# Kernel optimization log

Measured on AMD Instinct MI355X. Metric: run time of the kernel, lower is better.

Reference implementation:

```python
import jax, jax.numpy as jnp
import numpy as np

B, T, N, C = 4, 2048, 4, 1024   # batch, seq, expansion_rate, hidden_dim
A = 8                            # max_lora_adapters
SINKHORN_ITERS = 20
EPS = 1e-05


def _logit(x):
    x = jnp.clip(x, 1e-06, 1.0 - 1e-06)
    return jnp.log(x) - jnp.log(1.0 - x)


def setup_inputs() -> dict:
    key = jax.random.key(0)
    ks = jax.random.split(key, 12)
    nC = N * C
    x = jax.random.normal(ks[0], (B, T, N, C), dtype=jnp.float32)
    adapter_indices = jax.random.randint(ks[1], (B,), 0, A)
    # Learned parameters (perturbed from the identity init so gradients are non-trivial)
    input_norm_weight = 1.0 + 0.02 * jax.random.normal(ks[2], (A, nC), dtype=jnp.float32)
    phi_pre = 0.02 * jax.random.normal(ks[3], (A, nC, N), dtype=jnp.float32)
    phi_post = 0.02 * jax.random.normal(ks[4], (A, nC, N), dtype=jnp.float32)
    phi_res = 0.02 * jax.random.normal(ks[5], (A, nC, N * N), dtype=jnp.float32)
    b_pre = _logit(jnp.float32(1.0 / N)) + 0.1 * jax.random.normal(ks[6], (A, N), dtype=jnp.float32)
    b_post = 0.1 * jax.random.normal(ks[7], (A, N), dtype=jnp.float32)
    b_res = 10.0 * jnp.eye(N, dtype=jnp.float32) + jax.random.normal(ks[8], (A, N, N), dtype=jnp.float32)
    alpha_pre = 1.0 + 0.1 * jax.random.normal(ks[9], (A,), dtype=jnp.float32)
    alpha_post = 1.0 + 0.1 * jax.random.normal(ks[10], (A,), dtype=jnp.float32)
    alpha_res = 1.0 + 0.1 * jax.random.normal(ks[11], (A,), dtype=jnp.float32)
    return {
        "x": x,
        "input_norm_weight": input_norm_weight,
        "phi_pre": phi_pre, "phi_post": phi_post, "phi_res": phi_res,
        "b_pre": b_pre, "b_post": b_post, "b_res": b_res,
        "alpha_pre": alpha_pre, "alpha_post": alpha_post, "alpha_res": alpha_res,
        "adapter_indices": adapter_indices,
    }


def _sinkhorn_knopp(M, iters):
    M = jnp.exp(M)
    def step(_, mat):
        mat = mat / mat.sum(axis=-1, keepdims=True)
        mat = mat / mat.sum(axis=-2, keepdims=True)
        return mat
    return jax.lax.fori_loop(0, iters, step, M)


def reference(x, input_norm_weight, phi_pre, phi_post, phi_res,
              b_pre, b_post, b_res, alpha_pre, alpha_post, alpha_res,
              adapter_indices):
    Bb, Tt, n, Cc = x.shape
    idx = adapter_indices.astype(jnp.int32)
    x_flat = x.reshape(Bb, Tt, n * Cc)
    # adapter-indexed RMSNorm
    w = input_norm_weight[idx]                                  # [B, nC]
    rms = jnp.sqrt(jnp.mean(x_flat ** 2, axis=-1, keepdims=True) + EPS)
    x_norm = w[:, None, :] * x_flat / rms                       # [B, T, nC]
    # pre: input-dependent aggregation weights H_pre
    pre_logits = jnp.einsum('btd,bdn->btn', x_norm, phi_pre[idx])
    H_pre = jax.nn.sigmoid(alpha_pre[idx][:, None, None] * pre_logits + b_pre[idx][:, None, :])
    x_agg = (H_pre[..., None] * x).sum(axis=-2)                 # [B, T, C]
    output = x_agg                                              # identity block between pre and post
    # post: distribution weights H_post and doubly-stochastic mixing M
    post_logits = jnp.einsum('btd,bdn->btn', x_norm, phi_post[idx])
    H_post = 2.0 * jax.nn.sigmoid(alpha_post[idx][:, None, None] * post_logits + b_post[idx][:, None, :])
    res_logits = jnp.einsum('btd,bdm->btm', x_norm, phi_res[idx]).reshape(Bb, Tt, n, n)
    tilde_H_res = alpha_res[idx][:, None, None, None] * res_logits + b_res[idx][:, None, :, :]
    M = _sinkhorn_knopp(tilde_H_res, SINKHORN_ITERS)            # [B, T, n, n]
    y_dist = H_post[..., None] * output[..., None, :]           # [B, T, n, C]
    x_mixed = jnp.einsum('btij,btjc->btic', M, x)               # [B, T, n, C]
    return x_mixed + y_dist
```

## Files before the change

kernel.cpp:

```cpp
#include <hip/hip_runtime.h>


#define BT 8192
#define NC 4096
#define NC4 1024
#define NT 32
#define TD 128

__global__ __launch_bounds__(256) void lora_connector_kernel(
    const float* __restrict__ x,
    const float* __restrict__ inw,
    const float* __restrict__ phi_pre,
    const float* __restrict__ phi_post,
    const float* __restrict__ phi_res,
    const float* __restrict__ b_pre,
    const float* __restrict__ b_post,
    const float* __restrict__ b_res,
    const float* __restrict__ alpha_pre,
    const float* __restrict__ alpha_post,
    const float* __restrict__ alpha_res,
    const int*   __restrict__ adapter_indices,
    float* __restrict__ out)
{
    const int tid = threadIdx.x;
    const int g   = tid & 3;
    const int l   = tid >> 2;
    const int wvid= tid >> 6;
    const int ln  = tid & 63;
    const int dl  = tid & 127;
    const int half= tid >> 7;
    const int blk = blockIdx.x;
    const int b   = blk >> 9;
    const int idx = adapter_indices[b];

    const float4* __restrict__ pp4 = (const float4*)(phi_pre  + (size_t)idx * (NC * 4));
    const float4* __restrict__ po4 = (const float4*)(phi_post + (size_t)idx * (NC * 4));
    const float4* __restrict__ pr4 = (const float4*)(phi_res  + (size_t)idx * (NC * 16));
    const float*  __restrict__ inwp = inw + (size_t)idx * NC + dl;
    const float*  __restrict__ xb   = x + (size_t)(blk * 4) * NC + dl;

    __shared__ float4 tileL[2][768];
    __shared__ float red[4][4][14];

    const float4* sg[3];
    int sstr[3];
    #pragma unroll
    for (int i = 0; i < 3; ++i) {
        const int c = wvid * 3 + i;
        const float4* bp; int off, str;
        if (c < 4) {
            bp  = (c < 2) ? pp4 : po4;
            off = ((c & 1) << 6) + ln;
            str = TD;
        } else {
            const int k = c - 4;
            bp  = pr4;
            off = ((((k & 1) << 6) + ln) << 2) + (k >> 1);
            str = TD * 4;
        }
        sg[i] = bp + off;
        sstr[i] = str;
    }

    #define STAGE_TILE(MT, BF)                                                   \
    {                                                                            \
        _Pragma("unroll")                                                        \
        for (int i = 0; i < 3; ++i) {                                            \
            __builtin_amdgcn_global_load_lds(                                    \
                (const __attribute__((address_space(1))) void*)(sg[i] + (size_t)(MT) * sstr[i]), \
                (__attribute__((address_space(3))) void*)&tileL[BF][((wvid * 3 + i) << 6) + ln], \
                16, 0, 0);                                                       \
        }                                                                        \
    }

    STAGE_TILE(0, 0);

    float acc[12][4];
    float ss[4];
    #pragma unroll
    for (int j = 0; j < 12; ++j) {
        acc[j][0] = 0.0f; acc[j][1] = 0.0f; acc[j][2] = 0.0f; acc[j][3] = 0.0f;
    }
    ss[0] = ss[1] = ss[2] = ss[3] = 0.0f;

    float xn[4], wn;
    #pragma unroll
    for (int j = 0; j < 4; ++j) xn[j] = xb[j * NC];
    wn = inwp[0];

    const int ba = half * 384 + dl;

    #pragma unroll 1
    for (int m = 0; m < NT; ++m) {
        const int bf = m & 1;
        __syncthreads();
        if (m < NT - 1) STAGE_TILE(m + 1, bf ^ 1);

        const float wv = wn;
        float s[4];
        #pragma unroll
        for (int j = 0; j < 4; ++j) {
            const float xv = xn[j];
            s[j] = xv * wv;
            ss[j] = fmaf(xv, xv, ss[j]);
        }
        if (m < NT - 1) {
            #pragma unroll
            for (int j = 0; j < 4; ++j) xn[j] = xb[j * NC + (m + 1) * TD];
            wn = inwp[(m + 1) * TD];
        }

        const float4 a = tileL[bf][ba];
        const float4 p = tileL[bf][ba + 128];
        const float4 r = tileL[bf][ba + 256];
        #pragma unroll
        for (int j = 0; j < 4; ++j) {
            acc[0][j]  = fmaf(s[j], a.x, acc[0][j]);
            acc[1][j]  = fmaf(s[j], a.y, acc[1][j]);
            acc[2][j]  = fmaf(s[j], a.z, acc[2][j]);
            acc[3][j]  = fmaf(s[j], a.w, acc[3][j]);
            acc[4][j]  = fmaf(s[j], p.x, acc[4][j]);
            acc[5][j]  = fmaf(s[j], p.y, acc[5][j]);
            acc[6][j]  = fmaf(s[j], p.z, acc[6][j]);
            acc[7][j]  = fmaf(s[j], p.w, acc[7][j]);
            acc[8][j]  = fmaf(s[j], r.x, acc[8][j]);
            acc[9][j]  = fmaf(s[j], r.y, acc[9][j]);
            acc[10][j] = fmaf(s[j], r.z, acc[10][j]);
            acc[11][j] = fmaf(s[j], r.w, acc[11][j]);
        }
    }

    float t12[13];
    #define RED4(V0, V1, V2, V3, DST)                                   \
    {                                                                   \
        const float u0 = (V0) + __shfl_xor((V0), 1);                    \
        const float u1 = (V1) + __shfl_xor((V1), 1);                    \
        const float u2 = (V2) + __shfl_xor((V2), 1);                    \
        const float u3 = (V3) + __shfl_xor((V3), 1);                    \
        const float r0 = (ln & 1) ? u1 : u0;                            \
        const float r1 = (ln & 1) ? u3 : u2;                            \
        const float w0 = r0 + __shfl_xor(r0, 2);                        \
        const float w1 = r1 + __shfl_xor(r1, 2);                        \
        float tv = (ln & 2) ? w1 : w0;                                  \
        tv += __shfl_xor(tv, 4);  tv += __shfl_xor(tv, 8);              \
        tv += __shfl_xor(tv, 16); tv += __shfl_xor(tv, 32);             \
        (DST) = tv;                                                     \
    }
    #pragma unroll
    for (int j = 0; j < 12; ++j)
        RED4(acc[j][0], acc[j][1], acc[j][2], acc[j][3], t12[j]);
    RED4(ss[0], ss[1], ss[2], ss[3], t12[12]);
    #undef RED4

    if (ln < 4) {
        #pragma unroll
        for (int j = 0; j < 13; ++j) red[wvid][ln][j] = t12[j];
    }
    __syncthreads();
    float tot[25];
    #pragma unroll
    for (int j = 0; j < 12; ++j) {
        tot[j]      = red[0][g][j] + red[1][g][j];
        tot[12 + j] = red[2][g][j] + red[3][g][j];
    }
    tot[24] = red[0][g][12] + red[1][g][12];

    const float inv_rms = rsqrtf(tot[24] * (1.0f / 4096.0f) + 1e-5f);
    const float apre  = alpha_pre[idx];
    const float apost = alpha_post[idx];
    const float ares  = alpha_res[idx];

    float Hpre[4], Hpost[4];
    #pragma unroll
    for (int n = 0; n < 4; ++n) {
        const float zp = fmaf(apre,  tot[n]     * inv_rms, b_pre[idx * 4 + n]);
        Hpre[n]  = 1.0f / (1.0f + __expf(-zp));
        const float zq = fmaf(apost, tot[4 + n] * inv_rms, b_post[idx * 4 + n]);
        Hpost[n] = 2.0f / (1.0f + __expf(-zq));
    }

    const int s16 = ln >> 2;
    const int sj = s16 & 3;
    const int si = s16 >> 2;
    float Mv = __expf(fmaf(ares, tot[8 + si * 4 + sj] * inv_rms,
                           b_res[idx * 16 + si * 4 + sj]));
    #pragma unroll
    for (int it = 0; it < 20; ++it) {
        float rs = Mv + __shfl_xor(Mv, 4);
        rs += __shfl_xor(rs, 8);
        Mv *= __builtin_amdgcn_rcpf(rs);
        float cs = Mv + __shfl_xor(Mv, 16);
        cs += __shfl_xor(cs, 32);
        Mv *= __builtin_amdgcn_rcpf(cs);
    }

    float W[4][4];
    #pragma unroll
    for (int sq = 0; sq < 16; ++sq) {
        const float mm = __shfl(Mv, sq * 4 + g);
        W[sq >> 2][sq & 3] = fmaf(Hpost[sq >> 2], Hpre[sq & 3], mm);
    }

    const int tok = blk * 4 + g;
    const float4* __restrict__ x4p = (const float4*)x + (size_t)tok * NC4;
    float4* __restrict__ out4 = (float4*)out + (size_t)tok * NC4;
    #pragma unroll
    for (int k = 0; k < 4; ++k) {
        const int c4 = k * 64 + l;
        const float4 x0 = x4p[0 * 256 + c4];
        const float4 x1 = x4p[1 * 256 + c4];
        const float4 x2 = x4p[2 * 256 + c4];
        const float4 x3 = x4p[3 * 256 + c4];
        #pragma unroll
        for (int i = 0; i < 4; ++i) {
            float4 o;
            o.x = fmaf(W[i][0], x0.x, fmaf(W[i][1], x1.x, fmaf(W[i][2], x2.x, W[i][3] * x3.x)));
            o.y = fmaf(W[i][0], x0.y, fmaf(W[i][1], x1.y, fmaf(W[i][2], x2.y, W[i][3] * x3.y)));
            o.z = fmaf(W[i][0], x0.z, fmaf(W[i][1], x1.z, fmaf(W[i][2], x2.z, W[i][3] * x3.z)));
            o.w = fmaf(W[i][0], x0.w, fmaf(W[i][1], x1.w, fmaf(W[i][2], x2.w, W[i][3] * x3.w)));
            out4[i * 256 + c4] = o;
        }
    }
    #undef STAGE_TILE
}

extern "C" void kernel_launch(void* const* d_in, const int* in_sizes, int n_in,
                              void* d_out, int out_size, void* d_ws, size_t ws_size,
                              hipStream_t stream) {
    const float* x         = (const float*)d_in[0];
    const float* inw       = (const float*)d_in[1];
    const float* phi_pre   = (const float*)d_in[2];
    const float* phi_post  = (const float*)d_in[3];
    const float* phi_res   = (const float*)d_in[4];
    const float* b_pre     = (const float*)d_in[5];
    const float* b_post    = (const float*)d_in[6];
    const float* b_res     = (const float*)d_in[7];
    const float* alpha_pre = (const float*)d_in[8];
    const float* alpha_post= (const float*)d_in[9];
    const float* alpha_res = (const float*)d_in[10];
    const int*   adapter   = (const int*)d_in[11];
    float* out = (float*)d_out;

    dim3 grid(BT / 4);
    dim3 block(256);
    lora_connector_kernel<<<grid, block, 0, stream>>>(
        x, inw, phi_pre, phi_post, phi_res,
        b_pre, b_post, b_res,
        alpha_pre, alpha_post, alpha_res,
        adapter, out);
}
```

Measured before the change: 309.8 us.

## Double-buffer x/weight register prefetch two tiles ahead with explicit vmcnt waits

Restructures the GEMV-like reduction loop to prefetch the x and norm-weight values two tiles ahead into alternating register sets, and unrolls the loop by two. It replaces __syncthreads with an explicit s_waitcnt vmcnt(N) plus s_barrier, fenced by sched_barriers, so the LDS tile loads can stay in flight while other global loads are outstanding. The aim is to hide global-load latency better in this memory-bound phase. It relies on hand-counted vmcnt values being correct, which risks races if the compiler reorders or adds loads.

```diff
diff --git a/kernel.cpp b/kernel.cpp
--- a/kernel.cpp
+++ b/kernel.cpp
@@ -73,7 +73,12 @@
         }                                                                        \
     }
 
-    STAGE_TILE(0, 0);
+    #define XW_PRE(MT, XR, WR)                                                   \
+    {                                                                            \
+        _Pragma("unroll")                                                        \
+        for (int j = 0; j < 4; ++j) XR[j] = xb[j * NC + (MT) * TD];              \
+        WR = inwp[(MT) * TD];                                                    \
+    }
 
     float acc[12][4];
     float ss[4];
@@ -83,52 +88,59 @@
     }
     ss[0] = ss[1] = ss[2] = ss[3] = 0.0f;
 
-    float xn[4], wn;
-    #pragma unroll
-    for (int j = 0; j < 4; ++j) xn[j] = xb[j * NC];
-    wn = inwp[0];
-
     const int ba = half * 384 + dl;
 
+    float xnA[4], xnB[4], wnA, wnB;
+    STAGE_TILE(0, 0);
+    __builtin_amdgcn_sched_barrier(0);
+    XW_PRE(0, xnA, wnA);
+    XW_PRE(1, xnB, wnB);
+
+    #define ITER(M, BF, XC, WC, WAITN)                                           \
+    {                                                                            \
+        __builtin_amdgcn_sched_barrier(0);                                       \
+        asm volatile("s_waitcnt vmcnt(" #WAITN ")" ::: "memory");                \
+        __builtin_amdgcn_sched_barrier(0);                                       \
+        __builtin_amdgcn_s_barrier();                                            \
+        __builtin_amdgcn_sched_barrier(0);                                       \
+        if ((M) < NT - 1) STAGE_TILE((M) + 1, (BF) ^ 1);                         \
+        __builtin_amdgcn_sched_barrier(0);                                       \
+        float s[4];                                                              \
+        _Pragma("unroll")                                                        \
+        for (int j = 0; j < 4; ++j) {                                            \
+            const float xv = XC[j];                                              \
+            s[j] = xv * WC;                                                      \
+            ss[j] = fmaf(xv, xv, ss[j]);                                         \
+        }                                                                        \
+        if ((M) < NT - 2) XW_PRE((M) + 2, XC, WC);                               \
+        const float4 a = tileL[BF][ba];                                          \
+        const float4 p = tileL[BF][ba + 128];                                    \
+        const float4 r = tileL[BF][ba + 256];                                    \
+        _Pragma("unroll")                                                        \
+        for (int j = 0; j < 4; ++j) {                                            \
+            acc[0][j]  = fmaf(s[j], a.x, acc[0][j]);                             \
+            acc[1][j]  = fmaf(s[j], a.y, acc[1][j]);                             \
+            acc[2][j]  = fmaf(s[j], a.z, acc[2][j]);                             \
+            acc[3][j]  = fmaf(s[j], a.w, acc[3][j]);                             \
+            acc[4][j]  = fmaf(s[j], p.x, acc[4][j]);                             \
+            acc[5][j]  = fmaf(s[j], p.y, acc[5][j]);                             \
+            acc[6][j]  = fmaf(s[j], p.z, acc[6][j]);                             \
+            acc[7][j]  = fmaf(s[j], p.w, acc[7][j]);                             \
+            acc[8][j]  = fmaf(s[j], r.x, acc[8][j]);                             \
+            acc[9][j]  = fmaf(s[j], r.y, acc[9][j]);                             \
+            acc[10][j] = fmaf(s[j], r.z, acc[10][j]);                            \
+            acc[11][j] = fmaf(s[j], r.w, acc[11][j]);                            \
+        }                                                                        \
+    }
+
     #pragma unroll 1
-    for (int m = 0; m < NT; ++m) {
-        const int bf = m & 1;
-        __syncthreads();
-        if (m < NT - 1) STAGE_TILE(m + 1, bf ^ 1);
-
-        const float wv = wn;
-        float s[4];
-        #pragma unroll
-        for (int j = 0; j < 4; ++j) {
-            const float xv = xn[j];
-            s[j] = xv * wv;
-            ss[j] = fmaf(xv, xv, ss[j]);
-        }
-        if (m < NT - 1) {
-            #pragma unroll
-            for (int j = 0; j < 4; ++j) xn[j] = xb[j * NC + (m + 1) * TD];
-            wn = inwp[(m + 1) * TD];
-        }
-
-        const float4 a = tileL[bf][ba];
-        const float4 p = tileL[bf][ba + 128];
-        const float4 r = tileL[bf][ba + 256];
-        #pragma unroll
-        for (int j = 0; j < 4; ++j) {
-            acc[0][j]  = fmaf(s[j], a.x, acc[0][j]);
-            acc[1][j]  = fmaf(s[j], a.y, acc[1][j]);
-            acc[2][j]  = fmaf(s[j], a.z, acc[2][j]);
-            acc[3][j]  = fmaf(s[j], a.w, acc[3][j]);
-            acc[4][j]  = fmaf(s[j], p.x, acc[4][j]);
-            acc[5][j]  = fmaf(s[j], p.y, acc[5][j]);
-            acc[6][j]  = fmaf(s[j], p.z, acc[6][j]);
-            acc[7][j]  = fmaf(s[j], p.w, acc[7][j]);
-            acc[8][j]  = fmaf(s[j], r.x, acc[8][j]);
-            acc[9][j]  = fmaf(s[j], r.y, acc[9][j]);
-            acc[10][j] = fmaf(s[j], r.z, acc[10][j]);
-            acc[11][j] = fmaf(s[j], r.w, acc[11][j]);
-        }
-    }
+    for (int m = 0; m < NT - 2; m += 2) {
+        ITER(m,     0, xnA, wnA, 5);
+        ITER(m + 1, 1, xnB, wnB, 5);
+    }
+    ITER(NT - 2, 0, xnA, wnA, 5);
+    ITER(NT - 1, 1, xnB, wnB, 0);
+    #undef ITER
 
     float t12[13];
     #define RED4(V0, V1, V2, V3, DST)                                   \
@@ -222,6 +234,7 @@
         }
     }
     #undef STAGE_TILE
+    #undef XW_PRE
 }
 
 extern "C" void kernel_launch(void* const* d_in, const int* in_sizes, int n_in,
```

New measurement: 329.9 us. 6.5% more time.

## Split fused kernel into weight-computation and mixing kernels via workspace

Applied to the files above, without the earlier changes.

The single kernel is split in two. The first computes the per-token 4x4 mixing matrix (Sinkhorn result plus the Hpost·Hpre outer product) and writes it to a workspace buffer. A second kernel, launched with one block per token, reads x again and applies the mix. The aim is to decouple the reduction-heavy phase from the bandwidth-bound output phase so each runs with a better thread mapping. The cost is a second full read of x from memory (or from L2/MALL if it is still cached) and an extra kernel launch.

```diff
diff --git a/kernel.cpp b/kernel.cpp
--- a/kernel.cpp
+++ b/kernel.cpp
@@ -7,7 +7,7 @@
 #define NT 32
 #define TD 128
 
-__global__ __launch_bounds__(256) void lora_connector_kernel(
+__global__ __launch_bounds__(256) void lora_w_kernel(
     const float* __restrict__ x,
     const float* __restrict__ inw,
     const float* __restrict__ phi_pre,
@@ -20,11 +20,10 @@
     const float* __restrict__ alpha_post,
     const float* __restrict__ alpha_res,
     const int*   __restrict__ adapter_indices,
-    float* __restrict__ out)
+    float* __restrict__ wsf)
 {
     const int tid = threadIdx.x;
     const int g   = tid & 3;
-    const int l   = tid >> 2;
     const int wvid= tid >> 6;
     const int ln  = tid & 63;
     const int dl  = tid & 127;
@@ -194,34 +193,52 @@
         Mv *= __builtin_amdgcn_rcpf(cs);
     }
 
-    float W[4][4];
-    #pragma unroll
-    for (int sq = 0; sq < 16; ++sq) {
-        const float mm = __shfl(Mv, sq * 4 + g);
-        W[sq >> 2][sq & 3] = fmaf(Hpost[sq >> 2], Hpre[sq & 3], mm);
-    }
-
-    const int tok = blk * 4 + g;
-    const float4* __restrict__ x4p = (const float4*)x + (size_t)tok * NC4;
-    float4* __restrict__ out4 = (float4*)out + (size_t)tok * NC4;
-    #pragma unroll
-    for (int k = 0; k < 4; ++k) {
-        const int c4 = k * 64 + l;
-        const float4 x0 = x4p[0 * 256 + c4];
-        const float4 x1 = x4p[1 * 256 + c4];
-        const float4 x2 = x4p[2 * 256 + c4];
-        const float4 x3 = x4p[3 * 256 + c4];
-        #pragma unroll
-        for (int i = 0; i < 4; ++i) {
-            float4 o;
-            o.x = fmaf(W[i][0], x0.x, fmaf(W[i][1], x1.x, fmaf(W[i][2], x2.x, W[i][3] * x3.x)));
-            o.y = fmaf(W[i][0], x0.y, fmaf(W[i][1], x1.y, fmaf(W[i][2], x2.y, W[i][3] * x3.y)));
-            o.z = fmaf(W[i][0], x0.z, fmaf(W[i][1], x1.z, fmaf(W[i][2], x2.z, W[i][3] * x3.z)));
-            o.w = fmaf(W[i][0], x0.w, fmaf(W[i][1], x1.w, fmaf(W[i][2], x2.w, W[i][3] * x3.w)));
-            out4[i * 256 + c4] = o;
-        }
+    if (wvid == 0) {
+        const float hpo = (si == 0) ? Hpost[0] : (si == 1) ? Hpost[1]
+                        : (si == 2) ? Hpost[2] : Hpost[3];
+        const float hpr = (sj == 0) ? Hpre[0]  : (sj == 1) ? Hpre[1]
+                        : (sj == 2) ? Hpre[2]  : Hpre[3];
+        wsf[(size_t)blk * 64 + g * 16 + si * 4 + sj] = fmaf(hpo, hpr, Mv);
     }
     #undef STAGE_TILE
+}
+
+__global__ __launch_bounds__(256) void lora_mix_kernel(
+    const float* __restrict__ x,
+    const float* __restrict__ wsf,
+    float* __restrict__ out)
+{
+    const int tok = blockIdx.x;
+    const int c4  = threadIdx.x;
+
+    const float4* __restrict__ x4p = (const float4*)x   + (size_t)tok * NC4;
+    float4* __restrict__       out4 = (float4*)out      + (size_t)tok * NC4;
+    const float4* __restrict__ w4   = (const float4*)wsf + (size_t)tok * 4;
+
+    const float4 W0 = w4[0];
+    const float4 W1 = w4[1];
+    const float4 W2 = w4[2];
+    const float4 W3 = w4[3];
+
+    const float4 x0 = x4p[0 * 256 + c4];
+    const float4 x1 = x4p[1 * 256 + c4];
+    const float4 x2 = x4p[2 * 256 + c4];
+    const float4 x3 = x4p[3 * 256 + c4];
+
+    #define MIXROW(WR, DSTIDX)                                                    \
+    {                                                                             \
+        float4 o;                                                                 \
+        o.x = fmaf(WR.x, x0.x, fmaf(WR.y, x1.x, fmaf(WR.z, x2.x, WR.w * x3.x)));  \
+        o.y = fmaf(WR.x, x0.y, fmaf(WR.y, x1.y, fmaf(WR.z, x2.y, WR.w * x3.y)));  \
+        o.z = fmaf(WR.x, x0.z, fmaf(WR.y, x1.z, fmaf(WR.z, x2.z, WR.w * x3.z)));  \
+        o.w = fmaf(WR.x, x0.w, fmaf(WR.y, x1.w, fmaf(WR.z, x2.w, WR.w * x3.w)));  \
+        out4[(DSTIDX) * 256 + c4] = o;                                            \
+    }
+    MIXROW(W0, 0);
+    MIXROW(W1, 1);
+    MIXROW(W2, 2);
+    MIXROW(W3, 3);
+    #undef MIXROW
 }
 
 extern "C" void kernel_launch(void* const* d_in, const int* in_sizes, int n_in,
@@ -240,12 +257,13 @@
     const float* alpha_res = (const float*)d_in[10];
     const int*   adapter   = (const int*)d_in[11];
     float* out = (float*)d_out;
-
-    dim3 grid(BT / 4);
+    float* wsf = (float*)d_ws;
+
     dim3 block(256);
-    lora_connector_kernel<<<grid, block, 0, stream>>>(
+    lora_w_kernel<<<dim3(BT / 4), block, 0, stream>>>(
         x, inw, phi_pre, phi_post, phi_res,
         b_pre, b_post, b_res,
         alpha_pre, alpha_post, alpha_res,
-        adapter, out);
+        adapter, wsf);
+    lora_mix_kernel<<<dim3(BT), block, 0, stream>>>(x, wsf, out);
 }
```

Result: slower. 318.5 us (+2.8%).
